# Optimization experiments

Measured on AMD Instinct MI355X. Metric: run time of the kernel, lower is better.

Reference implementation:

```python
import jax, jax.numpy as jnp
import numpy as np

B, L, D_MODEL = 8, 2048, 512
D_STATE, EXPAND = 16, 2
D_INNER = D_MODEL * EXPAND
EPS = 1e-5


def setup_inputs() -> dict:
    key = jax.random.key(0)
    ks = jax.random.split(key, 16)
    s = 0.02
    return {
        "x": jax.random.normal(ks[0], (B, L, D_MODEL), jnp.float32),
        "norm_w": jnp.ones((D_MODEL,), jnp.float32),
        "norm_b": jnp.zeros((D_MODEL,), jnp.float32),
        "in_proj_w": jax.random.normal(ks[1], (2 * D_INNER, D_MODEL), jnp.float32) * s,
        "in_proj_b": jnp.zeros((2 * D_INNER,), jnp.float32),
        "conv_w": jax.random.normal(ks[2], (D_INNER, 1, 3), jnp.float32) * s,  # depthwise, groups=D_INNER
        "conv_b": jnp.zeros((D_INNER,), jnp.float32),
        "gru_w_ih": jax.random.normal(ks[3], (3 * D_STATE, D_INNER), jnp.float32) * s,
        "gru_w_hh": jax.random.normal(ks[4], (3 * D_STATE, D_STATE), jnp.float32) * s,
        "gru_b_ih": jnp.zeros((3 * D_STATE,), jnp.float32),
        "gru_b_hh": jnp.zeros((3 * D_STATE,), jnp.float32),
        "ssm_proj_w": jax.random.normal(ks[5], (D_INNER, D_STATE), jnp.float32) * s,
        "ssm_proj_b": jnp.zeros((D_INNER,), jnp.float32),
        "out_proj_w": jax.random.normal(ks[6], (D_MODEL, D_INNER), jnp.float32) * s,
        "out_proj_b": jnp.zeros((D_MODEL,), jnp.float32),
    }


def _silu(a):
    return a * jax.nn.sigmoid(a)


def reference(x, norm_w, norm_b, in_proj_w, in_proj_b, conv_w, conv_b,
              gru_w_ih, gru_w_hh, gru_b_ih, gru_b_hh,
              ssm_proj_w, ssm_proj_b, out_proj_w, out_proj_b):
    residual = x
    # LayerNorm over last dim
    mu = jnp.mean(x, axis=-1, keepdims=True)
    var = jnp.mean(jnp.square(x - mu), axis=-1, keepdims=True)
    xn = (x - mu) * jax.lax.rsqrt(var + EPS) * norm_w + norm_b
    # in_proj -> split into x_ and gate z
    xz = jnp.einsum("bld,ed->ble", xn, in_proj_w) + in_proj_b
    x_, z = jnp.split(xz, 2, axis=-1)  # each [B, L, D_INNER]
    # depthwise conv1d, kernel 3, pad 1
    xc = jax.lax.conv_general_dilated(
        x_.transpose(0, 2, 1), conv_w, window_strides=(1,), padding=[(1, 1)],
        dimension_numbers=("NCH", "OIH", "NCH"), feature_group_count=D_INNER)
    x_ = _silu((xc + conv_b[None, :, None]).transpose(0, 2, 1))  # [B, L, D_INNER]
    # GRU (batch_first), h0 = 0; PyTorch gate math
    xg = jnp.einsum("bld,gd->blg", x_, gru_w_ih) + gru_b_ih  # [B, L, 3H]
    def step(h, xt):
        gh = h @ gru_w_hh.T + gru_b_hh
        xr, xz_, xnn = jnp.split(xt, 3, axis=-1)
        hr, hz, hn = jnp.split(gh, 3, axis=-1)
        r = jax.nn.sigmoid(xr + hr)
        zt = jax.nn.sigmoid(xz_ + hz)
        n = jnp.tanh(xnn + r * hn)
        h_new = (1.0 - zt) * n + zt * h
        return h_new, h_new
    h0 = jnp.zeros((x.shape[0], D_STATE), x.dtype)
    _, ys = jax.lax.scan(step, h0, xg.transpose(1, 0, 2))
    y = ys.transpose(1, 0, 2)  # [B, L, D_STATE]
    y = jnp.einsum("bls,es->ble", y, ssm_proj_w) + ssm_proj_b
    y = y * _silu(z)
    y = jnp.einsum("ble,de->bld", y, out_proj_w) + out_proj_b
    return residual + y  # dropout = identity (eval mode)
```

## Files before the change

### kernel.cpp

```cpp
#include <hip/hip_runtime.h>
#include <hip/hip_bf16.h>

#define B_  8
#define L_  2048
#define DM  512
#define DI  1024
#define T_  (B_*L_)
#define EPSF 1e-5f
#define GCH 64

typedef short v8s __attribute__((ext_vector_type(8)));
typedef float v4f __attribute__((ext_vector_type(4)));
typedef float v2f __attribute__((ext_vector_type(2)));

__device__ __forceinline__ float bf2f(unsigned short h){
    union { unsigned int u; float f; } v; v.u = ((unsigned int)h) << 16; return v.f;
}
__device__ __forceinline__ unsigned short f2bf(float f){
    union { float f; unsigned int u; } v; v.f = f;
    unsigned int r = v.u + 0x7fffu + ((v.u >> 16) & 1u);
    return (unsigned short)(r >> 16);
}
__device__ __forceinline__ float sig_fast(float x){
    float e = __builtin_amdgcn_exp2f(x * -1.44269504089f);
    return __builtin_amdgcn_rcpf(1.f + e);
}
__device__ __forceinline__ float tanh_pade(float x){
    float t = x*x;
    float m = 27.f*x;
    float num = __builtin_fmaf(x, t, m);
    float den = __builtin_fmaf(9.f, t, 27.f);
    float v = num * __builtin_amdgcn_rcpf(den);
    return fminf(1.f, fmaxf(-1.f, v));
}
__device__ __forceinline__ float sig_pade(float x){
    return __builtin_fmaf(0.5f, tanh_pade(0.5f*x), 0.5f);
}
__device__ __forceinline__ v2f vfma2(v2f a, v2f b, v2f c){
#if __has_builtin(__builtin_elementwise_fma)
    return __builtin_elementwise_fma(a, b, c);
#else
    return (v2f){__builtin_fmaf(a.x,b.x,c.x), __builtin_fmaf(a.y,b.y,c.y)};
#endif
}

template<int CTRL>
__device__ __forceinline__ float dpp_rot(float x){
    int xi = __builtin_bit_cast(int, x);
    int r = __builtin_amdgcn_update_dpp(xi, xi, CTRL, 0xf, 0xf, false);
    return __builtin_bit_cast(float, r);
}

__device__ __forceinline__ void gload_lds16(const unsigned short* g, unsigned short* l){
    __builtin_amdgcn_global_load_lds(
        (const __attribute__((address_space(1))) unsigned int*)(const void*)g,
        (__attribute__((address_space(3))) unsigned int*)(void*)l,
        16, 0, 0);
}

__global__ void cvt_all_kernel(const float* __restrict__ in_w, const float* __restrict__ out_w,
                               const float* __restrict__ gih_w,
                               unsigned short* __restrict__ in_wb, unsigned short* __restrict__ out_wb,
                               unsigned short* __restrict__ gih_wb){
    int i = (blockIdx.x*256 + threadIdx.x)*4;
    const float* src; unsigned short* dst; int off;
    if(i < 1048576){ src = in_w;  dst = in_wb;  off = i; }
    else if(i < 1572864){ src = out_w; dst = out_wb; off = i - 1048576; }
    else {
        off = i - 1572864;
        int row = off >> 10;
        unsigned int p0 = 0, p1 = 0;
        if(row < 48){
            float4 f = *reinterpret_cast<const float4*>(gih_w + off);
            p0 = f2bf(f.x) | ((unsigned int)f2bf(f.y)<<16);
            p1 = f2bf(f.z) | ((unsigned int)f2bf(f.w)<<16);
        }
        uint2 pk = {p0,p1};
        *reinterpret_cast<uint2*>(gih_wb + off) = pk;
        return;
    }
    float4 f = *reinterpret_cast<const float4*>(src + off);
    unsigned int p0 = f2bf(f.x) | ((unsigned int)f2bf(f.y)<<16);
    unsigned int p1 = f2bf(f.z) | ((unsigned int)f2bf(f.w)<<16);
    uint2 pk = {p0,p1};
    *reinterpret_cast<uint2*>(dst + off) = pk;
}

__global__ void ln_kernel(const float* __restrict__ x, const float* __restrict__ w,
                          const float* __restrict__ b, unsigned short* __restrict__ xn){
    int row = blockIdx.x;
    int lane = threadIdx.x;
    const float* xr = x + (size_t)row*DM + lane*8;
    float4 v0 = *reinterpret_cast<const float4*>(xr);
    float4 v1 = *reinterpret_cast<const float4*>(xr + 4);
    float v[8] = {v0.x,v0.y,v0.z,v0.w,v1.x,v1.y,v1.z,v1.w};
    float s = 0.f, sq = 0.f;
    #pragma unroll
    for(int j=0;j<8;j++){ s += v[j]; sq += v[j]*v[j]; }
    #pragma unroll
    for(int o=32;o>0;o>>=1){ s += __shfl_xor(s,o); sq += __shfl_xor(sq,o); }
    float mu  = s*(1.f/DM);
    float var = sq*(1.f/DM) - mu*mu;
    float rs  = rsqrtf(var + EPSF);
    int c = lane*8;
    float4 w0 = *reinterpret_cast<const float4*>(w + c);
    float4 w1 = *reinterpret_cast<const float4*>(w + c + 4);
    float4 b0 = *reinterpret_cast<const float4*>(b + c);
    float4 b1 = *reinterpret_cast<const float4*>(b + c + 4);
    float wv[8] = {w0.x,w0.y,w0.z,w0.w,w1.x,w1.y,w1.z,w1.w};
    float bv[8] = {b0.x,b0.y,b0.z,b0.w,b1.x,b1.y,b1.z,b1.w};
    unsigned short o8[8];
    #pragma unroll
    for(int j=0;j<8;j++) o8[j] = f2bf((v[j]-mu)*rs*wv[j] + bv[j]);
    uint4 pk;
    pk.x = o8[0] | ((unsigned int)o8[1]<<16);
    pk.y = o8[2] | ((unsigned int)o8[3]<<16);
    pk.z = o8[4] | ((unsigned int)o8[5]<<16);
    pk.w = o8[6] | ((unsigned int)o8[7]<<16);
    *reinterpret_cast<uint4*>(xn + (size_t)row*DM + c) = pk;
}

template<int OUTMODE>
__global__ __launch_bounds__(256) void gemm_mfma(
    const unsigned short* __restrict__ A, int lda,
    const unsigned short* __restrict__ Bw, int K,
    const float* __restrict__ bias,
    const float* __restrict__ resid,
    void* __restrict__ Cout, int ldc)
{
    __shared__ __align__(16) unsigned short As[128][64];
    __shared__ __align__(16) unsigned short Bs[128][64];
    const int nwg = gridDim.x*gridDim.y;
    const int idx = blockIdx.y*gridDim.x + blockIdx.x;
    const int q8  = nwg >> 3;
    const int swz = (idx & 7)*q8 + (idx >> 3);
    const int m0 = (swz / gridDim.x) * 128;
    const int n0 = (swz % gridDim.x) * 128;
    const int tid = threadIdx.x;
    const int wave = tid >> 6;
    const int lane = tid & 63;
    const int wm = (wave >> 1) * 64, wn = (wave & 1) * 64;
    const int r16 = lane & 15, kc = lane >> 4;
    const int lrow = lane >> 3;
    const int lcs  = (((lane & 7) ^ lrow) << 3);
    const int rsw  = (r16 & 7) << 3;

    v4f acc[4][4];
    #pragma unroll
    for(int i=0;i<4;i++)
        #pragma unroll
        for(int j=0;j<4;j++) acc[i][j] = (v4f){0.f,0.f,0.f,0.f};

    for(int k0=0;k0<K;k0+=64){
        #pragma unroll
        for(int c=0;c<4;c++){
            int chunk = wave*4 + c;
            int row = chunk*8 + lrow;
            gload_lds16(A  + (size_t)(m0+row)*lda + k0 + lcs, &As[chunk*8][0]);
            gload_lds16(Bw + (size_t)(n0+row)*K   + k0 + lcs, &Bs[chunk*8][0]);
        }
        __syncthreads();
        #pragma unroll
        for(int kk=0;kk<2;kk++){
            v8s af[4], bfr[4];
            #pragma unroll
            for(int i=0;i<4;i++)
                af[i] = *reinterpret_cast<const v8s*>(&As[wm + i*16 + r16][(kk*32 + kc*8) ^ rsw]);
            #pragma unroll
            for(int j=0;j<4;j++)
                bfr[j] = *reinterpret_cast<const v8s*>(&Bs[wn + j*16 + r16][(kk*32 + kc*8) ^ rsw]);
            #pragma unroll
            for(int i=0;i<4;i++)
                #pragma unroll
                for(int j=0;j<4;j++)
                    acc[i][j] = __builtin_amdgcn_mfma_f32_16x16x32_bf16(af[i], bfr[j], acc[i][j], 0, 0, 0);
        }
        __syncthreads();
    }

    #pragma unroll
    for(int j=0;j<4;j++){
        int col = n0 + wn + j*16 + r16;
        float bj = bias[col];
        #pragma unroll
        for(int i=0;i<4;i++){
            int rowb = m0 + wm + i*16 + kc*4;
            #pragma unroll
            for(int r=0;r<4;r++){
                size_t row = (size_t)(rowb + r);
                float v = acc[i][j][r] + bj;
                if(OUTMODE == 0){
                    ((unsigned short*)Cout)[row*ldc + col] = f2bf(v);
                } else {
                    ((float*)Cout)[row*ldc + col] = v + resid[row*ldc + col];
                }
            }
        }
    }
}

__global__ __launch_bounds__(256) void gemm_xg(
    const unsigned short* __restrict__ xz,
    const float* __restrict__ cw, const float* __restrict__ cb,
    const unsigned short* __restrict__ Bw,
    const float* __restrict__ bias,
    float* __restrict__ xgT)
{
    __shared__ __align__(16) unsigned short As[128][72];
    __shared__ __align__(16) unsigned short Bs[64][72];
    const int m0 = blockIdx.x * 128;
    const int tid = threadIdx.x;
    const int wave = tid >> 6;
    const int lane = tid & 63;
    const int wm = (wave >> 1) * 64, wn = (wave & 1) * 32;
    const int r16 = lane & 15, kc = lane >> 4;
    const int srow = tid >> 3;
    const int scol = (tid & 7) * 8;

    v4f acc[4][2];
    #pragma unroll
    for(int i=0;i<4;i++){ acc[i][0] = (v4f){0,0,0,0}; acc[i][1] = (v4f){0,0,0,0}; }

    for(int k0=0;k0<1024;k0+=64){
        const int c = k0 + scol;
        float w0[8], w1[8], w2[8], cb8[8];
        #pragma unroll
        for(int j=0;j<8;j++){
            w0[j] = cw[(c+j)*3+0]; w1[j] = cw[(c+j)*3+1]; w2[j] = cw[(c+j)*3+2];
            cb8[j] = cb[c+j];
        }
        #pragma unroll
        for(int p=0;p<4;p++){
            int rr = srow + p*32;
            int t = m0 + rr;
            int ll = t & (L_-1);
            const unsigned short* rowp = xz + (size_t)t*2048 + c;
            uint4 uc = *reinterpret_cast<const uint4*>(rowp);
            uint4 up = {0,0,0,0}, un = {0,0,0,0};
            if(ll > 0)      up = *reinterpret_cast<const uint4*>(rowp - 2048);
            if(ll < L_-1)   un = *reinterpret_cast<const uint4*>(rowp + 2048);
            unsigned int ucw[4] = {uc.x,uc.y,uc.z,uc.w};
            unsigned int upw[4] = {up.x,up.y,up.z,up.w};
            unsigned int unw[4] = {un.x,un.y,un.z,un.w};
            unsigned short o8[8];
            #pragma unroll
            for(int j=0;j<8;j++){
                float curv = bf2f((unsigned short)((ucw[j>>1] >> ((j&1)*16)) & 0xffffu));
                float prvv = bf2f((unsigned short)((upw[j>>1] >> ((j&1)*16)) & 0xffffu));
                float nxtv = bf2f((unsigned short)((unw[j>>1] >> ((j&1)*16)) & 0xffffu));
                float v = __builtin_fmaf(w0[j], prvv, __builtin_fmaf(w1[j], curv, __builtin_fmaf(w2[j], nxtv, cb8[j])));
                o8[j] = f2bf(v * sig_fast(v));
            }
            uint4 pk;
            pk.x = o8[0] | ((unsigned int)o8[1]<<16);
            pk.y = o8[2] | ((unsigned int)o8[3]<<16);
            pk.z = o8[4] | ((unsigned int)o8[5]<<16);
            pk.w = o8[6] | ((unsigned int)o8[7]<<16);
            *reinterpret_cast<uint4*>(&As[rr][scol]) = pk;
        }
        #pragma unroll
        for(int p=0;p<2;p++){
            int rr = srow + p*32;
            uint4 bv = *reinterpret_cast<const uint4*>(Bw + (size_t)rr*1024 + k0 + scol);
            *reinterpret_cast<uint4*>(&Bs[rr][scol]) = bv;
        }
        __syncthreads();
        #pragma unroll
        for(int kk=0;kk<2;kk++){
            v8s af[4], bfr[2];
            #pragma unroll
            for(int i=0;i<4;i++)
                af[i] = *reinterpret_cast<const v8s*>(&As[wm + i*16 + r16][kk*32 + kc*8]);
            #pragma unroll
            for(int j=0;j<2;j++)
                bfr[j] = *reinterpret_cast<const v8s*>(&Bs[wn + j*16 + r16][kk*32 + kc*8]);
            #pragma unroll
            for(int i=0;i<4;i++)
                #pragma unroll
                for(int j=0;j<2;j++)
                    acc[i][j] = __builtin_amdgcn_mfma_f32_16x16x32_bf16(af[i], bfr[j], acc[i][j], 0, 0, 0);
        }
        __syncthreads();
    }
    #pragma unroll
    for(int j=0;j<2;j++){
        int col = wn + j*16 + r16;
        if(col < 48){
            float bj = bias[col];
            #pragma unroll
            for(int i=0;i<4;i++){
                int rowb = m0 + wm + i*16 + kc*4;
                int bb = rowb >> 11, ll = rowb & 2047;
                float4 v4 = {acc[i][j][0]+bj, acc[i][j][1]+bj, acc[i][j][2]+bj, acc[i][j][3]+bj};
                *reinterpret_cast<float4*>(xgT + ((size_t)bb*48 + col)*2048 + ll) = v4;
            }
        }
    }
}

__global__ __launch_bounds__(64) void gru_kernel(
    const float* __restrict__ xgT, const float* __restrict__ whh,
    const float* __restrict__ bhh, float* __restrict__ yT){
    __shared__ __align__(16) float ystage[4][16][68];
    const int tid = threadIdx.x;
    const int s = tid & 15;
    const int sl = tid >> 4;
    const int scan = blockIdx.x*4 + sl;
    const int c = scan >> 3;
    const int b = scan & 7;
    const int warm_groups = (c == 0) ? 0 : 16;
    const int ngroups = warm_groups + 16;
    const int tload = c*GCH - warm_groups*4;

    int mk = __builtin_amdgcn_update_dpp(s, s, 0x121, 0xf, 0xf, false);
    int dir = (mk == ((s+15)&15)) ? 15 : 1;

    v2f w2r[8], w2z[8], w2n[8];
    #pragma unroll
    for(int k=0;k<8;k++){
        int jA = (s + k*dir) & 15;
        int jB = (s + (k+8)*dir) & 15;
        w2r[k] = (v2f){ whh[(     s)*16 + jA], whh[(     s)*16 + jB] };
        w2z[k] = (v2f){ whh[(16 + s)*16 + jA], whh[(16 + s)*16 + jB] };
        w2n[k] = (v2f){ whh[(32 + s)*16 + jA], whh[(32 + s)*16 + jB] };
    }
    const float br = bhh[s], bz = bhh[16+s], bn = bhh[32+s];
    const float* xr_ = xgT + ((size_t)b*48 +      s)*L_ + tload;
    const float* xz_ = xgT + ((size_t)b*48 + 16 + s)*L_ + tload;
    const float* xn_ = xgT + ((size_t)b*48 + 32 + s)*L_ + tload;

    union F4 { float4 v; float a[4]; };
    F4 fr[4], fz[4], fn[4];
    #pragma unroll
    for(int g=0; g<4; g++){
        fr[g].v = *reinterpret_cast<const float4*>(xr_ + g*4);
        fz[g].v = *reinterpret_cast<const float4*>(xz_ + g*4);
        fn[g].v = *reinterpret_cast<const float4*>(xn_ + g*4);
        fr[g].a[0]+=br; fr[g].a[1]+=br; fr[g].a[2]+=br; fr[g].a[3]+=br;
        fz[g].a[0]+=bz; fz[g].a[1]+=bz; fz[g].a[2]+=bz; fz[g].a[3]+=bz;
    }
    v2f h2[8];
    #pragma unroll
    for(int k=0;k<8;k++) h2[k] = (v2f){0.f, 0.f};

    for(int G=0; G<ngroups; ++G){
        int qq = G & 3;
        int nx = G + 4; if(nx > ngroups-1) nx = ngroups-1;
        float4 pr = *reinterpret_cast<const float4*>(xr_ + nx*4);
        float4 pz = *reinterpret_cast<const float4*>(xz_ + nx*4);
        float4 pn = *reinterpret_cast<const float4*>(xn_ + nx*4);
        F4 ho;
        #pragma unroll
        for(int j=0;j<4;j++){
            v2f ar0 = w2r[0]*h2[0], ar1 = w2r[1]*h2[1], ar2 = w2r[2]*h2[2], ar3 = w2r[3]*h2[3];
            v2f az0 = w2z[0]*h2[0], az1 = w2z[1]*h2[1], az2 = w2z[2]*h2[2], az3 = w2z[3]*h2[3];
            v2f an0 = w2n[0]*h2[0], an1 = w2n[1]*h2[1], an2 = w2n[2]*h2[2], an3 = w2n[3]*h2[3];
            ar0 = vfma2(w2r[4],h2[4],ar0); ar1 = vfma2(w2r[5],h2[5],ar1);
            ar2 = vfma2(w2r[6],h2[6],ar2); ar3 = vfma2(w2r[7],h2[7],ar3);
            az0 = vfma2(w2z[4],h2[4],az0); az1 = vfma2(w2z[5],h2[5],az1);
            az2 = vfma2(w2z[6],h2[6],az2); az3 = vfma2(w2z[7],h2[7],az3);
            an0 = vfma2(w2n[4],h2[4],an0); an1 = vfma2(w2n[5],h2[5],an1);
            an2 = vfma2(w2n[6],h2[6],an2); an3 = vfma2(w2n[7],h2[7],an3);
            v2f arp = (ar0+ar1)+(ar2+ar3);
            v2f azp = (az0+az1)+(az2+az3);
            v2f anp = (an0+an1)+(an2+an3);
            float gr = arp.x + arp.y;
            float gz = azp.x + azp.y;
            float gn = anp.x + anp.y;
            float r   = sig_pade(fr[qq].a[j] + gr);
            float zt  = sig_pade(fz[qq].a[j] + gz);
            float pre = __builtin_fmaf(r, bn + gn, fn[qq].a[j]);
            float n   = tanh_pade(pre);
            float h0  = h2[0].x;
            float hnew = __builtin_fmaf(zt, h0 - n, n);
            ho.a[j] = hnew;
            h2[0] = (v2f){ hnew,                 dpp_rot<0x128>(hnew) };
            h2[1] = (v2f){ dpp_rot<0x121>(hnew), dpp_rot<0x129>(hnew) };
            h2[2] = (v2f){ dpp_rot<0x122>(hnew), dpp_rot<0x12A>(hnew) };
            h2[3] = (v2f){ dpp_rot<0x123>(hnew), dpp_rot<0x12B>(hnew) };
            h2[4] = (v2f){ dpp_rot<0x124>(hnew), dpp_rot<0x12C>(hnew) };
            h2[5] = (v2f){ dpp_rot<0x125>(hnew), dpp_rot<0x12D>(hnew) };
            h2[6] = (v2f){ dpp_rot<0x126>(hnew), dpp_rot<0x12E>(hnew) };
            h2[7] = (v2f){ dpp_rot<0x127>(hnew), dpp_rot<0x12F>(hnew) };
        }
        if(G >= warm_groups){
            *reinterpret_cast<float4*>(&ystage[sl][s][(G - warm_groups)*4]) = ho.v;
        }
        pr.x+=br; pr.y+=br; pr.z+=br; pr.w+=br;
        pz.x+=bz; pz.y+=bz; pz.z+=bz; pz.w+=bz;
        fr[qq].v = pr; fz[qq].v = pz; fn[qq].v = pn;
    }
    __syncthreads();
    #pragma unroll
    for(int k=0;k<16;k++){
        int slot = tid + k*64;
        int row = slot >> 4, c4 = slot & 15;
        int fsl = row >> 4, fs = row & 15;
        int fscan = blockIdx.x*4 + fsl;
        int fc = fscan >> 3, fb = fscan & 7;
        float4 v = *reinterpret_cast<const float4*>(&ystage[0][0][0] + (size_t)row*68 + c4*4);
        *reinterpret_cast<float4*>(yT + ((size_t)fb*16 + fs)*L_ + fc*GCH + c4*4) = v;
    }
}

__global__ __launch_bounds__(256) void gated_kernel(
    const float* __restrict__ yT, const float* __restrict__ sw,
    const float* __restrict__ sb, unsigned short* __restrict__ xz){
    const int tid = threadIdx.x;
    const int e = tid * 4;
    float w[4][16]; float sb4[4];
    #pragma unroll
    for(int j=0;j<4;j++){
        sb4[j] = sb[e+j];
        float4 a0 = *reinterpret_cast<const float4*>(sw + (size_t)(e+j)*16);
        float4 a1 = *reinterpret_cast<const float4*>(sw + (size_t)(e+j)*16 + 4);
        float4 a2 = *reinterpret_cast<const float4*>(sw + (size_t)(e+j)*16 + 8);
        float4 a3 = *reinterpret_cast<const float4*>(sw + (size_t)(e+j)*16 + 12);
        w[j][0]=a0.x; w[j][1]=a0.y; w[j][2]=a0.z; w[j][3]=a0.w;
        w[j][4]=a1.x; w[j][5]=a1.y; w[j][6]=a1.z; w[j][7]=a1.w;
        w[j][8]=a2.x; w[j][9]=a2.y; w[j][10]=a2.z; w[j][11]=a2.w;
        w[j][12]=a3.x; w[j][13]=a3.y; w[j][14]=a3.z; w[j][15]=a3.w;
    }
    for(int t = blockIdx.x; t < T_; t += gridDim.x){
        const int bb = t >> 11, ll = t & 2047;
        float yv[16];
        #pragma unroll
        for(int k=0;k<16;k++) yv[k] = yT[((size_t)bb*16 + k)*L_ + ll];
        uint2 zz = *reinterpret_cast<const uint2*>(xz + (size_t)t*2048 + 1024 + e);
        float zv[4] = {bf2f(zz.x&0xffffu), bf2f(zz.x>>16), bf2f(zz.y&0xffffu), bf2f(zz.y>>16)};
        unsigned short o[4];
        #pragma unroll
        for(int j=0;j<4;j++){
            float a0=sb4[j], a1=0.f, a2=0.f, a3=0.f;
            #pragma unroll
            for(int k=0;k<16;k+=4){
                a0 = __builtin_fmaf(w[j][k  ], yv[k  ], a0);
                a1 = __builtin_fmaf(w[j][k+1], yv[k+1], a1);
                a2 = __builtin_fmaf(w[j][k+2], yv[k+2], a2);
                a3 = __builtin_fmaf(w[j][k+3], yv[k+3], a3);
            }
            float a = (a0+a1)+(a2+a3);
            float sz = zv[j]*sig_fast(zv[j]);
            o[j] = f2bf(a*sz);
        }
        unsigned int p0 = o[0] | ((unsigned int)o[1]<<16);
        unsigned int p1 = o[2] | ((unsigned int)o[3]<<16);
        uint2 pk = {p0,p1};
        *reinterpret_cast<uint2*>(xz + (size_t)t*2048 + e) = pk;
    }
}

extern "C" void kernel_launch(void* const* d_in, const int* in_sizes, int n_in,
                              void* d_out, int out_size, void* d_ws, size_t ws_size,
                              hipStream_t stream) {
    const float* x        = (const float*)d_in[0];
    const float* norm_w   = (const float*)d_in[1];
    const float* norm_b   = (const float*)d_in[2];
    const float* in_w     = (const float*)d_in[3];
    const float* in_b     = (const float*)d_in[4];
    const float* conv_w   = (const float*)d_in[5];
    const float* conv_b   = (const float*)d_in[6];
    const float* gih_w    = (const float*)d_in[7];
    const float* ghh_w    = (const float*)d_in[8];
    const float* gih_b    = (const float*)d_in[9];
    const float* ghh_b    = (const float*)d_in[10];
    const float* ssm_w    = (const float*)d_in[11];
    const float* ssm_b    = (const float*)d_in[12];
    const float* out_w    = (const float*)d_in[13];
    const float* out_b    = (const float*)d_in[14];
    float* out = (float*)d_out;

    char* w = (char*)d_ws;
    unsigned short* xn    = (unsigned short*)(w);
    unsigned short* xz    = (unsigned short*)(w + 16777216);
    float*          xg    = (float*)(w + 117440512);
    float*          yb    = (float*)(w + 120586240);
    unsigned short* in_wb = (unsigned short*)(w + 121634816);
    unsigned short* out_wb= (unsigned short*)(w + 123731968);
    unsigned short* gih_wb= (unsigned short*)(w + 124780544);

    cvt_all_kernel<<<1600, 256, 0, stream>>>(in_w, out_w, gih_w, in_wb, out_wb, gih_wb);
    ln_kernel<<<T_, 64, 0, stream>>>(x, norm_w, norm_b, xn);
    gemm_mfma<0><<<dim3(2048/128, T_/128), 256, 0, stream>>>(xn, DM, in_wb, DM, in_b, nullptr, xz, 2*DI);
    gemm_xg<<<T_/128, 256, 0, stream>>>(xz, conv_w, conv_b, gih_wb, gih_b, xg);
    gru_kernel<<<64, 64, 0, stream>>>(xg, ghh_w, ghh_b, yb);
    gated_kernel<<<1024, 256, 0, stream>>>(yb, ssm_w, ssm_b, xz);
    gemm_mfma<2><<<dim3(DM/128, T_/128), 256, 0, stream>>>(xz, 2*DI, out_wb, DI, out_b, x, out, DM);
}
```

Baseline: 203.1 us.

## Double-buffer LDS tiles in GEMM and vectorize epilogue via swapped MFMA operands

The MFMA GEMM now double-buffers its A/B tiles in shared memory, issuing the next k-tile's global-to-LDS loads before computing the current one, and needs one barrier per iteration instead of two. Swapping the MFMA operands transposes each accumulator fragment, so every lane holds four consecutive columns. The epilogue then writes packed bf16x4 or float4 stores and reads the residual as float4, with bias preloaded as float4. Shared memory per block doubles, which can lower occupancy.

```diff
diff --git a/kernel.cpp b/kernel.cpp
--- a/kernel.cpp
+++ b/kernel.cpp
@@ -128,8 +128,8 @@
     const float* __restrict__ resid,
     void* __restrict__ Cout, int ldc)
 {
-    __shared__ __align__(16) unsigned short As[128][64];
-    __shared__ __align__(16) unsigned short Bs[128][64];
+    __shared__ __align__(16) unsigned short As[2][128][64];
+    __shared__ __align__(16) unsigned short Bs[2][128][64];
     const int nwg = gridDim.x*gridDim.y;
     const int idx = blockIdx.y*gridDim.x + blockIdx.x;
     const int q8  = nwg >> 3;
@@ -145,58 +145,81 @@
     const int lcs  = (((lane & 7) ^ lrow) << 3);
     const int rsw  = (r16 & 7) << 3;
 
+    float4 bias4[4];
+    #pragma unroll
+    for(int j=0;j<4;j++)
+        bias4[j] = *reinterpret_cast<const float4*>(bias + n0 + wn + j*16 + kc*4);
+
     v4f acc[4][4];
     #pragma unroll
     for(int i=0;i<4;i++)
         #pragma unroll
         for(int j=0;j<4;j++) acc[i][j] = (v4f){0.f,0.f,0.f,0.f};
 
-    for(int k0=0;k0<K;k0+=64){
-        #pragma unroll
-        for(int c=0;c<4;c++){
-            int chunk = wave*4 + c;
-            int row = chunk*8 + lrow;
-            gload_lds16(A  + (size_t)(m0+row)*lda + k0 + lcs, &As[chunk*8][0]);
-            gload_lds16(Bw + (size_t)(n0+row)*K   + k0 + lcs, &Bs[chunk*8][0]);
-        }
+    const int nk = K >> 6;
+    #define STAGE(k0_, bsel_) {                                                   \
+        _Pragma("unroll")                                                         \
+        for(int c=0;c<4;c++){                                                     \
+            int chunk = wave*4 + c;                                               \
+            int row = chunk*8 + lrow;                                             \
+            gload_lds16(A  + (size_t)(m0+row)*lda + (k0_) + lcs, &As[bsel_][chunk*8][0]); \
+            gload_lds16(Bw + (size_t)(n0+row)*K   + (k0_) + lcs, &Bs[bsel_][chunk*8][0]); \
+        }                                                                         \
+    }
+    #define COMPUTE(bsel_) {                                                      \
+        _Pragma("unroll")                                                         \
+        for(int kk=0;kk<2;kk++){                                                  \
+            v8s af[4], bfr[4];                                                    \
+            _Pragma("unroll")                                                     \
+            for(int i=0;i<4;i++)                                                  \
+                af[i] = *reinterpret_cast<const v8s*>(&As[bsel_][wm + i*16 + r16][(kk*32 + kc*8) ^ rsw]); \
+            _Pragma("unroll")                                                     \
+            for(int j=0;j<4;j++)                                                  \
+                bfr[j] = *reinterpret_cast<const v8s*>(&Bs[bsel_][wn + j*16 + r16][(kk*32 + kc*8) ^ rsw]); \
+            _Pragma("unroll")                                                     \
+            for(int i=0;i<4;i++)                                                  \
+                _Pragma("unroll")                                                 \
+                for(int j=0;j<4;j++)                                              \
+                    acc[i][j] = __builtin_amdgcn_mfma_f32_16x16x32_bf16(bfr[j], af[i], acc[i][j], 0, 0, 0); \
+        }                                                                         \
+    }
+
+    STAGE(0, 0);
+    __syncthreads();
+    int cur = 0;
+    for(int ki=0; ki<nk-1; ki++){
+        STAGE((ki+1)*64, cur^1);
+        COMPUTE(cur);
         __syncthreads();
-        #pragma unroll
-        for(int kk=0;kk<2;kk++){
-            v8s af[4], bfr[4];
-            #pragma unroll
-            for(int i=0;i<4;i++)
-                af[i] = *reinterpret_cast<const v8s*>(&As[wm + i*16 + r16][(kk*32 + kc*8) ^ rsw]);
-            #pragma unroll
-            for(int j=0;j<4;j++)
-                bfr[j] = *reinterpret_cast<const v8s*>(&Bs[wn + j*16 + r16][(kk*32 + kc*8) ^ rsw]);
-            #pragma unroll
-            for(int i=0;i<4;i++)
-                #pragma unroll
-                for(int j=0;j<4;j++)
-                    acc[i][j] = __builtin_amdgcn_mfma_f32_16x16x32_bf16(af[i], bfr[j], acc[i][j], 0, 0, 0);
-        }
-        __syncthreads();
-    }
-
-    #pragma unroll
-    for(int j=0;j<4;j++){
-        int col = n0 + wn + j*16 + r16;
-        float bj = bias[col];
-        #pragma unroll
-        for(int i=0;i<4;i++){
-            int rowb = m0 + wm + i*16 + kc*4;
-            #pragma unroll
-            for(int r=0;r<4;r++){
-                size_t row = (size_t)(rowb + r);
-                float v = acc[i][j][r] + bj;
-                if(OUTMODE == 0){
-                    ((unsigned short*)Cout)[row*ldc + col] = f2bf(v);
-                } else {
-                    ((float*)Cout)[row*ldc + col] = v + resid[row*ldc + col];
-                }
+        cur ^= 1;
+    }
+    COMPUTE(cur);
+
+    #pragma unroll
+    for(int i=0;i<4;i++){
+        size_t row = (size_t)(m0 + wm + i*16 + r16);
+        #pragma unroll
+        for(int j=0;j<4;j++){
+            int c4 = n0 + wn + j*16 + kc*4;
+            float4 b4 = bias4[j];
+            float v0 = acc[i][j][0] + b4.x;
+            float v1 = acc[i][j][1] + b4.y;
+            float v2 = acc[i][j][2] + b4.z;
+            float v3 = acc[i][j][3] + b4.w;
+            if(OUTMODE == 0){
+                unsigned int p0 = f2bf(v0) | ((unsigned int)f2bf(v1)<<16);
+                unsigned int p1 = f2bf(v2) | ((unsigned int)f2bf(v3)<<16);
+                uint2 pk = {p0, p1};
+                *reinterpret_cast<uint2*>((unsigned short*)Cout + row*ldc + c4) = pk;
+            } else {
+                float4 rv = *reinterpret_cast<const float4*>(resid + row*ldc + c4);
+                float4 ov = {v0+rv.x, v1+rv.y, v2+rv.z, v3+rv.w};
+                *reinterpret_cast<float4*>((float*)Cout + row*ldc + c4) = ov;
             }
         }
     }
+    #undef STAGE
+    #undef COMPUTE
 }
 
 __global__ __launch_bounds__(256) void gemm_xg(
```

After: 207.4 us. 2.1% more time.
